# Kernel tuning notes

Measured on AMD Instinct MI355X. Metric: run time of the kernel, lower is better.

The kernel has to match this reference:

```python
import jax, jax.numpy as jnp
import numpy as np

N = 50000       # nodes
E = 1250000     # edges
DIM = 64
H = 16
DPH = DIM // H  # 4
LN_EPS = 1e-5


def setup_inputs() -> dict:
    key = jax.random.key(0)
    ks = jax.random.split(key, 10)
    return {
        "node_feat": jax.random.normal(ks[0], (N, DIM), jnp.float32),
        "edge_feat": jax.random.normal(ks[1], (E, H, DPH), jnp.float32),
        "node_vec": jax.random.normal(ks[2], (N, 3, DIM), jnp.float32),
        "radial": jax.random.uniform(ks[3], (E,), jnp.float32),
        "ln_g": jnp.ones((DIM,), jnp.float32),
        "ln_b": jnp.zeros((DIM,), jnp.float32),
        "qkv_w": jax.random.normal(ks[4], (DIM, 3 * DIM), jnp.float32) / np.sqrt(DIM).astype(np.float32),
        "qkv_b": jnp.zeros((3 * DIM,), jnp.float32),
        "vec_w": jax.random.normal(ks[5], (DIM, 2 * DIM), jnp.float32) / np.sqrt(DIM).astype(np.float32),
        "out_w": jax.random.normal(ks[6], (DIM, 2 * DIM), jnp.float32) / np.sqrt(DIM).astype(np.float32),
        "out_b": jnp.zeros((2 * DIM,), jnp.float32),
        "row": jax.random.randint(ks[7], (E,), 0, N, jnp.int32),
        "col": jax.random.randint(ks[8], (E,), 0, N, jnp.int32),
        "natoms": N,
    }


def reference(node_feat, edge_feat, node_vec, radial, ln_g, ln_b,
              qkv_w, qkv_b, vec_w, out_w, out_b, row, col, natoms):
    # LayerNorm (biased variance, as torch)
    mu = jnp.mean(node_feat, axis=-1, keepdims=True)
    var = jnp.mean(jnp.square(node_feat - mu), axis=-1, keepdims=True)
    x = (node_feat - mu) * jax.lax.rsqrt(var + LN_EPS) * ln_g + ln_b

    # QKV projection -> [N, H, 3*DPH], split
    qkv = (x @ qkv_w + qkv_b).reshape(-1, H, 3 * DPH)
    q = qkv[..., :DPH]
    k = qkv[..., DPH:2 * DPH]
    v = qkv[..., 2 * DPH:]

    # Gather by edge indices, gated dot-product attention per edge  [E, H]
    attn = jax.nn.gelu(jnp.sum(q[row] * k[col], axis=-1), approximate=False) * radial[:, None]

    # Equivariant vector gate  [N, DIM]
    iv = node_vec @ vec_w  # [N, 3, 2*DIM]
    input_dot = jnp.sum(iv[..., :DIM] * iv[..., DIM:], axis=-2)

    # Edge messages and scatter-add into nodes
    m = v[col] * edge_feat * attn[..., None]          # [E, H, DPH]
    m_agg = jax.ops.segment_sum(m, row, num_segments=natoms)  # [N, H, DPH]
    m_agg = m_agg.reshape(natoms, DIM)

    out = m_agg @ out_w + out_b                        # [N, 2*DIM]
    return input_dot * out[..., :DIM] + out[..., DIM:]
```

## Files before the change

kernel.cpp:

```cpp
#include <hip/hip_runtime.h>
#include <math.h>

#define DIM 64
#define NW 4
#define NPB 4

__device__ __forceinline__ float waveReduceSum(float v) {
    #pragma unroll
    for (int off = 1; off < 64; off <<= 1)
        v += __shfl_xor(v, off, 64);
    return v;
}

__global__ __launch_bounds__(256) void qkv_kernel(
    const float* __restrict__ node_feat,
    const float* __restrict__ ln_g, const float* __restrict__ ln_b,
    const float* __restrict__ qkv_w, const float* __restrict__ qkv_b,
    float* __restrict__ q, float* __restrict__ k, float* __restrict__ v,
    int N)
{
    __shared__ float  wlds[64 * 192];
    __shared__ float4 xs[NW][NPB][16];
    const int wave = threadIdx.x >> 6, lane = threadIdx.x & 63;

    for (int idx = threadIdx.x; idx < 64 * 192; idx += 256) {
        int d = idx / 192, j = idx - d * 192;
        int jj = j & 63, sec = j >> 6;
        int c = 12 * (jj >> 2) + (jj & 3) + 4 * sec;
        wlds[idx] = qkv_w[d * 192 + c];
    }
    const int c0 = 12 * (lane >> 2) + (lane & 3);
    const float b0 = qkv_b[c0], b1 = qkv_b[c0 + 4], b2 = qkv_b[c0 + 8];
    const float gg = ln_g[lane], bb = ln_b[lane];
    __syncthreads();

    const int nstride = gridDim.x * NW * NPB;
    for (int n0 = (blockIdx.x * NW + wave) * NPB; n0 < N; n0 += nstride) {
        const int cnt = min(NPB, N - n0);
        float acc0[NPB], acc1[NPB], acc2[NPB];
        #pragma unroll
        for (int i = 0; i < NPB; ++i) {
            acc0[i] = b0; acc1[i] = b1; acc2[i] = b2;
            if (i < cnt) {
                float nf = node_feat[(size_t)(n0 + i) * DIM + lane];
                float mu = waveReduceSum(nf) * (1.0f / 64.0f);
                float dv = nf - mu;
                float var = waveReduceSum(dv * dv) * (1.0f / 64.0f);
                float x = dv * rsqrtf(var + 1e-5f) * gg + bb;
                ((float*)&xs[wave][i][0])[lane] = x;
            }
        }
        #pragma unroll 4
        for (int d4 = 0; d4 < 16; ++d4) {
            float4 xv[NPB];
            #pragma unroll
            for (int i = 0; i < NPB; ++i) xv[i] = xs[wave][i][d4];
            #pragma unroll
            for (int u = 0; u < 4; ++u) {
                int d = d4 * 4 + u;
                float w0 = wlds[d * 192 + lane];
                float w1 = wlds[d * 192 + lane + 64];
                float w2 = wlds[d * 192 + lane + 128];
                #pragma unroll
                for (int i = 0; i < NPB; ++i) {
                    float xd = (&xv[i].x)[u];
                    acc0[i] = fmaf(xd, w0, acc0[i]);
                    acc1[i] = fmaf(xd, w1, acc1[i]);
                    acc2[i] = fmaf(xd, w2, acc2[i]);
                }
            }
        }
        #pragma unroll
        for (int i = 0; i < NPB; ++i) if (i < cnt) {
            size_t off = (size_t)(n0 + i) * DIM + lane;
            q[off] = acc0[i]; k[off] = acc1[i]; v[off] = acc2[i];
        }
    }
}

__global__ __launch_bounds__(256) void vec_kernel(
    const float* __restrict__ node_vec,
    const float* __restrict__ vec_w,
    float* __restrict__ input_dot,
    float* __restrict__ m_agg,
    int N)
{
    __shared__ float  vlds[64 * 128];
    __shared__ float4 nvs[NW][NPB][3][16];
    const int wave = threadIdx.x >> 6, lane = threadIdx.x & 63;

    for (int idx = threadIdx.x; idx < 64 * 128; idx += 256)
        vlds[idx] = vec_w[idx];
    __syncthreads();

    const int nstride = gridDim.x * NW * NPB;
    for (int n0 = (blockIdx.x * NW + wave) * NPB; n0 < N; n0 += nstride) {
        const int cnt = min(NPB, N - n0);
        float a0[NPB][3], a1[NPB][3];
        #pragma unroll
        for (int i = 0; i < NPB; ++i) {
            #pragma unroll
            for (int s = 0; s < 3; ++s) {
                a0[i][s] = 0.f; a1[i][s] = 0.f;
                if (i < cnt)
                    ((float*)&nvs[wave][i][s][0])[lane] =
                        node_vec[((size_t)(n0 + i) * 3 + s) * DIM + lane];
            }
        }
        #pragma unroll 2
        for (int d4 = 0; d4 < 16; ++d4) {
            #pragma unroll
            for (int u = 0; u < 4; ++u) {
                int d = d4 * 4 + u;
                float w0 = vlds[d * 128 + lane];
                float w1 = vlds[d * 128 + lane + 64];
                #pragma unroll
                for (int i = 0; i < NPB; ++i) {
                    #pragma unroll
                    for (int s = 0; s < 3; ++s) {
                        float nv = ((float*)&nvs[wave][i][s][d4])[u];
                        a0[i][s] = fmaf(nv, w0, a0[i][s]);
                        a1[i][s] = fmaf(nv, w1, a1[i][s]);
                    }
                }
            }
        }
        #pragma unroll
        for (int i = 0; i < NPB; ++i) if (i < cnt) {
            size_t off = (size_t)(n0 + i) * DIM + lane;
            input_dot[off] = a0[i][0] * a1[i][0] + a0[i][1] * a1[i][1]
                           + a0[i][2] * a1[i][2];
            m_agg[off] = 0.0f;
        }
    }
}

__global__ __launch_bounds__(256) void edge_kernel(
    const float* __restrict__ q,
    const float* __restrict__ k,
    const float* __restrict__ v,
    const float* __restrict__ edge_feat,
    const float* __restrict__ radial,
    const int* __restrict__ row,
    const int* __restrict__ col,
    float* __restrict__ m_agg,
    int E)
{
    const int wave = threadIdx.x >> 6, lane = threadIdx.x & 63;
    const int e = blockIdx.x * NW + wave;
    if (e >= E) return;

    const int r = row[e];
    const int c = col[e];

    float qd = q[(size_t)r * DIM + lane];
    float kd = k[(size_t)c * DIM + lane];
    float p = qd * kd;
    p += __shfl_xor(p, 1, 64);
    p += __shfl_xor(p, 2, 64);

    float g = 0.5f * p * (1.0f + erff(p * 0.70710678118654752f));
    float a = g * radial[e];

    float ef = __builtin_nontemporal_load(&edge_feat[(size_t)e * DIM + lane]);
    float m = v[(size_t)c * DIM + lane] * ef * a;
    atomicAdd(&m_agg[(size_t)r * DIM + lane], m);
}

__global__ __launch_bounds__(256) void out_kernel(
    const float* __restrict__ m_agg,
    const float* __restrict__ input_dot,
    const float* __restrict__ out_w,
    const float* __restrict__ out_b,
    float* __restrict__ result,
    int N)
{
    __shared__ float  olds[64 * 128];
    __shared__ float4 ms[NW][NPB][16];
    const int wave = threadIdx.x >> 6, lane = threadIdx.x & 63;

    for (int idx = threadIdx.x; idx < 64 * 128; idx += 256)
        olds[idx] = out_w[idx];
    const float ob0 = out_b[lane], ob1 = out_b[lane + 64];
    __syncthreads();

    const int nstride = gridDim.x * NW * NPB;
    for (int n0 = (blockIdx.x * NW + wave) * NPB; n0 < N; n0 += nstride) {
        const int cnt = min(NPB, N - n0);
        float o0[NPB], o1[NPB];
        #pragma unroll
        for (int i = 0; i < NPB; ++i) {
            o0[i] = ob0; o1[i] = ob1;
            if (i < cnt)
                ((float*)&ms[wave][i][0])[lane] =
                    m_agg[(size_t)(n0 + i) * DIM + lane];
        }
        #pragma unroll 4
        for (int d4 = 0; d4 < 16; ++d4) {
            float4 mv[NPB];
            #pragma unroll
            for (int i = 0; i < NPB; ++i) mv[i] = ms[wave][i][d4];
            #pragma unroll
            for (int u = 0; u < 4; ++u) {
                int d = d4 * 4 + u;
                float w0 = olds[d * 128 + lane];
                float w1 = olds[d * 128 + lane + 64];
                #pragma unroll
                for (int i = 0; i < NPB; ++i) {
                    float md = (&mv[i].x)[u];
                    o0[i] = fmaf(md, w0, o0[i]);
                    o1[i] = fmaf(md, w1, o1[i]);
                }
            }
        }
        #pragma unroll
        for (int i = 0; i < NPB; ++i) if (i < cnt) {
            size_t off = (size_t)(n0 + i) * DIM + lane;
            result[off] = input_dot[off] * o0[i] + o1[i];
        }
    }
}

extern "C" void kernel_launch(void* const* d_in, const int* in_sizes, int n_in,
                              void* d_out, int out_size, void* d_ws, size_t ws_size,
                              hipStream_t stream)
{
    const float* node_feat = (const float*)d_in[0];
    const float* edge_feat = (const float*)d_in[1];
    const float* node_vec  = (const float*)d_in[2];
    const float* radial    = (const float*)d_in[3];
    const float* ln_g      = (const float*)d_in[4];
    const float* ln_b      = (const float*)d_in[5];
    const float* qkv_w     = (const float*)d_in[6];
    const float* qkv_b     = (const float*)d_in[7];
    const float* vec_w     = (const float*)d_in[8];
    const float* out_w     = (const float*)d_in[9];
    const float* out_b     = (const float*)d_in[10];
    const int*   row       = (const int*)d_in[11];
    const int*   col       = (const int*)d_in[12];

    const int N = in_sizes[0] / DIM;
    const int E = in_sizes[3];

    float* ws    = (float*)d_ws;
    float* q     = ws;
    float* k     = q    + (size_t)N * DIM;
    float* v     = k    + (size_t)N * DIM;
    float* idot  = v    + (size_t)N * DIM;
    float* m_agg = idot + (size_t)N * DIM;

    const int grid_nodes = 768;
    const int eblk = (E + NW - 1) / NW;

    qkv_kernel<<<grid_nodes, 256, 0, stream>>>(node_feat, ln_g, ln_b,
                                               qkv_w, qkv_b, q, k, v, N);
    vec_kernel<<<grid_nodes, 256, 0, stream>>>(node_vec, vec_w, idot, m_agg, N);
    edge_kernel<<<eblk, 256, 0, stream>>>(q, k, v, edge_feat, radial,
                                          row, col, m_agg, E);
    out_kernel<<<grid_nodes, 256, 0, stream>>>(m_agg, idot, out_w, out_b,
                                               (float*)d_out, N);
}
```

Before: 857.7 us.

## Bucket edges by destination row and aggregate per node without atomics

```diff
diff --git a/kernel.cpp b/kernel.cpp
--- a/kernel.cpp
+++ b/kernel.cpp
@@ -4,6 +4,8 @@
 #define DIM 64
 #define NW 4
 #define NPB 4
+#define CAP 64
+#define OVCAP 65536
 
 __device__ __forceinline__ float waveReduceSum(float v) {
     #pragma unroll
@@ -83,11 +85,15 @@
     const float* __restrict__ vec_w,
     float* __restrict__ input_dot,
     float* __restrict__ m_agg,
+    int* __restrict__ deg,
+    int* __restrict__ ovcnt,
     int N)
 {
     __shared__ float  vlds[64 * 128];
     __shared__ float4 nvs[NW][NPB][3][16];
     const int wave = threadIdx.x >> 6, lane = threadIdx.x & 63;
+
+    if (blockIdx.x == 0 && threadIdx.x == 0) *ovcnt = 0;
 
     for (int idx = threadIdx.x; idx < 64 * 128; idx += 256)
         vlds[idx] = vec_w[idx];
@@ -131,11 +137,93 @@
             input_dot[off] = a0[i][0] * a1[i][0] + a0[i][1] * a1[i][1]
                            + a0[i][2] * a1[i][2];
             m_agg[off] = 0.0f;
-        }
-    }
-}
-
-__global__ __launch_bounds__(256) void edge_kernel(
+            if (lane == 0) deg[n0 + i] = 0;
+        }
+    }
+}
+
+__global__ __launch_bounds__(256) void scatter_kernel(
+    const int* __restrict__ row,
+    const int* __restrict__ col,
+    int* __restrict__ deg,
+    int* __restrict__ perm,
+    int* __restrict__ ovcnt,
+    int* __restrict__ ovlist,
+    const float* __restrict__ q, const float* __restrict__ k,
+    const float* __restrict__ v,
+    const float* __restrict__ edge_feat, const float* __restrict__ radial,
+    float* __restrict__ m_agg,
+    int E)
+{
+    for (int e = blockIdx.x * 256 + threadIdx.x; e < E; e += gridDim.x * 256) {
+        int r = row[e];
+        int slot = atomicAdd(&deg[r], 1);
+        if (slot < CAP) {
+            perm[(size_t)r * CAP + slot] = e;
+        } else {
+            int o = atomicAdd(ovcnt, 1);
+            if (o < OVCAP) {
+                ovlist[o] = e;
+            } else {
+                int c = col[e];
+                float rad = radial[e];
+                float ah[16];
+                #pragma unroll
+                for (int h = 0; h < 16; ++h) {
+                    float p = 0.f;
+                    #pragma unroll
+                    for (int t = 0; t < 4; ++t)
+                        p += q[(size_t)r * DIM + h * 4 + t] *
+                             k[(size_t)c * DIM + h * 4 + t];
+                    float g = 0.5f * p * (1.0f + erff(p * 0.70710678118654752f));
+                    ah[h] = g * rad;
+                }
+                for (int d = 0; d < DIM; ++d)
+                    atomicAdd(&m_agg[(size_t)r * DIM + d],
+                              v[(size_t)c * DIM + d] *
+                              edge_feat[(size_t)e * DIM + d] * ah[d >> 2]);
+            }
+        }
+    }
+}
+
+__global__ __launch_bounds__(256) void agg_kernel(
+    const float* __restrict__ q,
+    const float* __restrict__ k,
+    const float* __restrict__ v,
+    const float* __restrict__ edge_feat,
+    const float* __restrict__ radial,
+    const int* __restrict__ col,
+    const int* __restrict__ perm,
+    const int* __restrict__ deg,
+    float* __restrict__ m_agg,
+    int N)
+{
+    const int wave = threadIdx.x >> 6, lane = threadIdx.x & 63;
+    for (int n = blockIdx.x * NW + wave; n < N; n += gridDim.x * NW) {
+        int cn = min(deg[n], CAP);
+        const int* pr = perm + (size_t)n * CAP;
+        const float qd = q[n * DIM + lane];
+        float acc = 0.0f;
+        #pragma unroll 2
+        for (int j = 0; j < cn; ++j) {
+            int e = pr[j];
+            int c = col[e];
+            float kd = k[c * DIM + lane];
+            float vd = v[c * DIM + lane];
+            float ef = __builtin_nontemporal_load(&edge_feat[e * DIM + lane]);
+            float rad = radial[e];
+            float p = qd * kd;
+            p += __shfl_xor(p, 1, 64);
+            p += __shfl_xor(p, 2, 64);
+            float g = 0.5f * p * (1.0f + erff(p * 0.70710678118654752f));
+            acc = fmaf(vd * ef, g * rad, acc);
+        }
+        m_agg[n * DIM + lane] += acc;
+    }
+}
+
+__global__ __launch_bounds__(256) void ovf_kernel(
     const float* __restrict__ q,
     const float* __restrict__ k,
     const float* __restrict__ v,
@@ -143,28 +231,23 @@
     const float* __restrict__ radial,
     const int* __restrict__ row,
     const int* __restrict__ col,
-    float* __restrict__ m_agg,
-    int E)
-{
-    const int wave = threadIdx.x >> 6, lane = threadIdx.x & 63;
-    const int e = blockIdx.x * NW + wave;
-    if (e >= E) return;
-
-    const int r = row[e];
-    const int c = col[e];
-
-    float qd = q[(size_t)r * DIM + lane];
-    float kd = k[(size_t)c * DIM + lane];
-    float p = qd * kd;
-    p += __shfl_xor(p, 1, 64);
-    p += __shfl_xor(p, 2, 64);
-
-    float g = 0.5f * p * (1.0f + erff(p * 0.70710678118654752f));
-    float a = g * radial[e];
-
-    float ef = __builtin_nontemporal_load(&edge_feat[(size_t)e * DIM + lane]);
-    float m = v[(size_t)c * DIM + lane] * ef * a;
-    atomicAdd(&m_agg[(size_t)r * DIM + lane], m);
+    const int* __restrict__ ovcnt,
+    const int* __restrict__ ovlist,
+    float* __restrict__ m_agg)
+{
+    const int wave = threadIdx.x >> 6, lane = threadIdx.x & 63;
+    const int ovn = min(*ovcnt, OVCAP);
+    for (int i = blockIdx.x * NW + wave; i < ovn; i += gridDim.x * NW) {
+        int e = ovlist[i];
+        int r = row[e], c = col[e];
+        float p = q[r * DIM + lane] * k[c * DIM + lane];
+        p += __shfl_xor(p, 1, 64);
+        p += __shfl_xor(p, 2, 64);
+        float g = 0.5f * p * (1.0f + erff(p * 0.70710678118654752f));
+        float a = g * radial[e];
+        float m = v[c * DIM + lane] * edge_feat[(size_t)e * DIM + lane] * a;
+        atomicAdd(&m_agg[r * DIM + lane], m);
+    }
 }
 
 __global__ __launch_bounds__(256) void out_kernel(
@@ -248,15 +331,24 @@
     float* v     = k    + (size_t)N * DIM;
     float* idot  = v    + (size_t)N * DIM;
     float* m_agg = idot + (size_t)N * DIM;
+    int*   deg    = (int*)(m_agg + (size_t)N * DIM);
+    int*   ovcnt  = deg + N;
+    int*   ovlist = ovcnt + 1;
+    int*   perm   = ovlist + OVCAP;
 
     const int grid_nodes = 768;
-    const int eblk = (E + NW - 1) / NW;
+    const int grid_agg   = (N + NW - 1) / NW;
 
     qkv_kernel<<<grid_nodes, 256, 0, stream>>>(node_feat, ln_g, ln_b,
                                                qkv_w, qkv_b, q, k, v, N);
-    vec_kernel<<<grid_nodes, 256, 0, stream>>>(node_vec, vec_w, idot, m_agg, N);
-    edge_kernel<<<eblk, 256, 0, stream>>>(q, k, v, edge_feat, radial,
-                                          row, col, m_agg, E);
+    vec_kernel<<<grid_nodes, 256, 0, stream>>>(node_vec, vec_w, idot, m_agg,
+                                               deg, ovcnt, N);
+    scatter_kernel<<<2048, 256, 0, stream>>>(row, col, deg, perm, ovcnt, ovlist,
+                                             q, k, v, edge_feat, radial, m_agg, E);
+    agg_kernel<<<grid_agg, 256, 0, stream>>>(q, k, v, edge_feat, radial,
+                                             col, perm, deg, m_agg, N);
+    ovf_kernel<<<256, 256, 0, stream>>>(q, k, v, edge_feat, radial,
+                                        row, col, ovcnt, ovlist, m_agg);
     out_kernel<<<grid_nodes, 256, 0, stream>>>(m_agg, idot, out_w, out_b,
                                                (float*)d_out, N);
 }
```

New measurement: 871.3 us. Within noise of the previous version (+1.6%).

## Bucket edges by destination node and aggregate per node without atomics

Applied to the files above, without the earlier changes.

```diff
diff --git a/kernel.cpp b/kernel.cpp
--- a/kernel.cpp
+++ b/kernel.cpp
@@ -4,6 +4,7 @@
 #define DIM 64
 #define NW 4
 #define NPB 4
+#define CAP 64
 
 __device__ __forceinline__ float waveReduceSum(float v) {
     #pragma unroll
@@ -82,8 +83,15 @@
     const float* __restrict__ node_vec,
     const float* __restrict__ vec_w,
     float* __restrict__ input_dot,
+    const int* __restrict__ row,
+    const int* __restrict__ col,
+    int* __restrict__ deg,
+    int2* __restrict__ perm2,
+    const float* __restrict__ q, const float* __restrict__ k,
+    const float* __restrict__ v,
+    const float* __restrict__ edge_feat, const float* __restrict__ radial,
     float* __restrict__ m_agg,
-    int N)
+    int N, int E)
 {
     __shared__ float  vlds[64 * 128];
     __shared__ float4 nvs[NW][NPB][3][16];
@@ -130,41 +138,110 @@
             size_t off = (size_t)(n0 + i) * DIM + lane;
             input_dot[off] = a0[i][0] * a1[i][0] + a0[i][1] * a1[i][1]
                            + a0[i][2] * a1[i][2];
-            m_agg[off] = 0.0f;
-        }
-    }
-}
-
-__global__ __launch_bounds__(256) void edge_kernel(
+        }
+    }
+
+    for (int e = blockIdx.x * 256 + threadIdx.x; e < E; e += gridDim.x * 256) {
+        int r = row[e];
+        int slot = atomicAdd(&deg[r], 1);
+        if (slot < CAP) {
+            perm2[(size_t)r * CAP + slot] = make_int2(e, col[e]);
+        } else {
+            int c = col[e];
+            float rad = radial[e];
+            #pragma unroll 1
+            for (int h = 0; h < 16; ++h) {
+                float p = 0.f;
+                #pragma unroll
+                for (int t = 0; t < 4; ++t)
+                    p += q[(size_t)r * DIM + h * 4 + t] *
+                         k[(size_t)c * DIM + h * 4 + t];
+                float g = 0.5f * p * (1.0f + erff(p * 0.70710678118654752f));
+                float a = g * rad;
+                #pragma unroll
+                for (int t = 0; t < 4; ++t) {
+                    int d = h * 4 + t;
+                    atomicAdd(&m_agg[(size_t)r * DIM + d],
+                              v[(size_t)c * DIM + d] *
+                              edge_feat[(size_t)e * DIM + d] * a);
+                }
+            }
+        }
+    }
+}
+
+__device__ __forceinline__ void edge_body(
+    int j, int2 ec, float radv, float qd,
+    const float* __restrict__ k, const float* __restrict__ v,
+    const float* __restrict__ edge_feat, int lane, float& acc)
+{
+    int   e   = __shfl(ec.x, j, 64);
+    int   c   = __shfl(ec.y, j, 64);
+    float rad = __shfl(radv, j, 64);
+    float kd = k[(size_t)c * DIM + lane];
+    float vd = v[(size_t)c * DIM + lane];
+    float ef = __builtin_nontemporal_load(&edge_feat[(size_t)e * DIM + lane]);
+    float p = qd * kd;
+    p += __shfl_xor(p, 1, 64);
+    p += __shfl_xor(p, 2, 64);
+    float g = 0.5f * p * (1.0f + erff(p * 0.70710678118654752f));
+    acc = fmaf(vd * ef, g * rad, acc);
+}
+
+__global__ __launch_bounds__(256) void agg_kernel(
     const float* __restrict__ q,
     const float* __restrict__ k,
     const float* __restrict__ v,
     const float* __restrict__ edge_feat,
     const float* __restrict__ radial,
-    const int* __restrict__ row,
-    const int* __restrict__ col,
+    const int2* __restrict__ perm2,
+    const int* __restrict__ deg,
     float* __restrict__ m_agg,
-    int E)
+    int N)
 {
     const int wave = threadIdx.x >> 6, lane = threadIdx.x & 63;
-    const int e = blockIdx.x * NW + wave;
-    if (e >= E) return;
-
-    const int r = row[e];
-    const int c = col[e];
-
-    float qd = q[(size_t)r * DIM + lane];
-    float kd = k[(size_t)c * DIM + lane];
-    float p = qd * kd;
-    p += __shfl_xor(p, 1, 64);
-    p += __shfl_xor(p, 2, 64);
-
-    float g = 0.5f * p * (1.0f + erff(p * 0.70710678118654752f));
-    float a = g * radial[e];
-
-    float ef = __builtin_nontemporal_load(&edge_feat[(size_t)e * DIM + lane]);
-    float m = v[(size_t)c * DIM + lane] * ef * a;
-    atomicAdd(&m_agg[(size_t)r * DIM + lane], m);
+    const int nstride = gridDim.x * NW * 2;
+    for (int n0 = (blockIdx.x * NW + wave) * 2; n0 < N; n0 += nstride) {
+        const int nA = n0, nB = n0 + 1;
+        const bool hasB = nB < N;
+        const int dAraw = deg[nA];
+        const int dBraw = hasB ? deg[nB] : 0;
+        const int cnA = min(dAraw, CAP);
+        const int cnB = min(dBraw, CAP);
+        int2 ecA = make_int2(0, 0), ecB = make_int2(0, 0);
+        float radA = 0.f, radB = 0.f;
+        if (lane < cnA) {
+            ecA = perm2[(size_t)nA * CAP + lane];
+            radA = radial[ecA.x];
+        }
+        if (lane < cnB) {
+            ecB = perm2[(size_t)nB * CAP + lane];
+            radB = radial[ecB.x];
+        }
+        const float qdA = q[(size_t)nA * DIM + lane];
+        const float qdB = hasB ? q[(size_t)nB * DIM + lane] : 0.f;
+        float accA = 0.f, accB = 0.f;
+
+        const int cmin = min(cnA, cnB);
+        #pragma unroll 2
+        for (int j = 0; j < cmin; ++j) {
+            edge_body(j, ecA, radA, qdA, k, v, edge_feat, lane, accA);
+            edge_body(j, ecB, radB, qdB, k, v, edge_feat, lane, accB);
+        }
+        #pragma unroll 4
+        for (int j = cmin; j < cnA; ++j)
+            edge_body(j, ecA, radA, qdA, k, v, edge_feat, lane, accA);
+        #pragma unroll 4
+        for (int j = cmin; j < cnB; ++j)
+            edge_body(j, ecB, radB, qdB, k, v, edge_feat, lane, accB);
+
+        if (dAraw > CAP) accA += m_agg[(size_t)nA * DIM + lane];
+        m_agg[(size_t)nA * DIM + lane] = accA;
+        if (hasB) {
+            if (dBraw > CAP) accB += m_agg[(size_t)nB * DIM + lane];
+            m_agg[(size_t)nB * DIM + lane] = accB;
+        }
+    }
 }
 
 __global__ __launch_bounds__(256) void out_kernel(
@@ -248,15 +325,23 @@
     float* v     = k    + (size_t)N * DIM;
     float* idot  = v    + (size_t)N * DIM;
     float* m_agg = idot + (size_t)N * DIM;
+    int2*  perm2 = (int2*)(m_agg + (size_t)N * DIM);
+    int*   deg   = (int*)(perm2 + (size_t)N * CAP);
 
     const int grid_nodes = 768;
-    const int eblk = (E + NW - 1) / NW;
+    const int grid_agg   = (N + NW * 2 - 1) / (NW * 2);
+
+    hipMemsetAsync(m_agg, 0, (size_t)N * DIM * sizeof(float), stream);
+    hipMemsetAsync(deg,   0, (size_t)N * sizeof(int), stream);
 
     qkv_kernel<<<grid_nodes, 256, 0, stream>>>(node_feat, ln_g, ln_b,
                                                qkv_w, qkv_b, q, k, v, N);
-    vec_kernel<<<grid_nodes, 256, 0, stream>>>(node_vec, vec_w, idot, m_agg, N);
-    edge_kernel<<<eblk, 256, 0, stream>>>(q, k, v, edge_feat, radial,
-                                          row, col, m_agg, E);
+    vec_kernel<<<grid_nodes, 256, 0, stream>>>(node_vec, vec_w, idot,
+                                               row, col, deg, perm2,
+                                               q, k, v, edge_feat, radial,
+                                               m_agg, N, E);
+    agg_kernel<<<grid_agg, 256, 0, stream>>>(q, k, v, edge_feat, radial,
+                                             perm2, deg, m_agg, N);
     out_kernel<<<grid_nodes, 256, 0, stream>>>(m_agg, idot, out_w, out_b,
                                                (float*)d_out, N);
 }
```

Result: faster. 766.6 us (-10.6%).
